# Performance work log

Hardware: AMD Instinct MI355X
Metric: run time of the kernel (lower is better)

## Reference

```python
import jax, jax.numpy as jnp
import numpy as np

B, T, D, H = 4, 2048, 1024, 16
DH = D // H          # 64
HALF = DH // 2       # 32


def _rope_tables(T, half, base=10000.0):
    inv_freq = 1.0 / (base ** (np.arange(half, dtype=np.float32) / half))
    t = np.arange(T, dtype=np.float32)
    ang = np.outer(t, inv_freq)                       # [T, half]
    cos = jnp.asarray(np.cos(ang))[None, None]        # [1,1,T,half]
    sin = jnp.asarray(np.sin(ang))[None, None]
    return cos, sin


def setup_inputs() -> dict:
    key = jax.random.key(0)
    kx, kq, kp = jax.random.split(key, 3)
    cos, sin = _rope_tables(T, HALF)
    return {
        "x": jax.random.normal(kx, (B, T, D), dtype=jnp.float32),
        "cos": cos,
        "sin": sin,
        "W_qkv": jax.random.normal(kq, (3 * D, D), dtype=jnp.float32) * (D ** -0.5),
        "W_proj": jax.random.normal(kp, (D, D), dtype=jnp.float32) * (D ** -0.5),
    }


def _apply_rope(q, k, cos, sin):
    # q,k: [B,H,T,dh]; cos,sin: [1,1,T,dh/2]
    t = q.shape[2]
    c, s = cos[:, :, :t, :], sin[:, :, :t, :]
    h = q.shape[-1] // 2
    q1, q2 = q[..., :h], q[..., h:]
    k1, k2 = k[..., :h], k[..., h:]
    q_rot = jnp.concatenate([q1 * c - q2 * s, q1 * s + q2 * c], axis=-1)
    k_rot = jnp.concatenate([k1 * c - k2 * s, k1 * s + k2 * c], axis=-1)
    return q_rot, k_rot


def reference(x, cos, sin, W_qkv, W_proj):
    Bb, Tt, C = x.shape
    qkv = x @ W_qkv.T                                 # [B,T,3C]
    q, k, v = jnp.split(qkv, 3, axis=2)
    # [B,T,C] -> [B,H,T,dh]
    q = q.reshape(Bb, Tt, H, DH).transpose(0, 2, 1, 3)
    k = k.reshape(Bb, Tt, H, DH).transpose(0, 2, 1, 3)
    v = v.reshape(Bb, Tt, H, DH).transpose(0, 2, 1, 3)
    q, k = _apply_rope(q, k, cos, sin)
    w = jnp.einsum("bhqd,bhkd->bhqk", q, k) * (DH ** -0.5)
    causal = jnp.tril(jnp.ones((Tt, Tt), dtype=bool))
    w = jnp.where(causal, w, -jnp.inf)
    w = jax.nn.softmax(w.astype(jnp.float32), axis=-1).astype(x.dtype)
    out = jnp.einsum("bhqk,bhkd->bhqd", w, v)
    # XSA: subtract self-value contribution (diagonal attention weight)
    self_w = jnp.diagonal(w, axis1=-2, axis2=-1)[..., None]  # [B,H,T,1]
    out = out - self_w * v
    out = out.transpose(0, 2, 1, 3).reshape(Bb, Tt, C)
    return out @ W_proj.T
```

## Files before the change

kernel.cpp:

```cpp
#include <hip/hip_runtime.h>

constexpr int Tq = 2048;
constexpr int Dq = 1024;

typedef __bf16 bf16x8 __attribute__((ext_vector_type(8)));
typedef float f32x4 __attribute__((ext_vector_type(4)));
typedef _Float16 f16;
typedef f16 f16x4 __attribute__((ext_vector_type(4)));
typedef f16 f16x8v __attribute__((ext_vector_type(8)));
typedef unsigned short u16;
typedef u16 u16x4 __attribute__((ext_vector_type(4)));
typedef u16 u16x8 __attribute__((ext_vector_type(8)));

__device__ __forceinline__ u16 f2bf(float f) {
    unsigned int u = __float_as_uint(f);
    u += 0x7fffu + ((u >> 16) & 1u);
    return (u16)(u >> 16);
}
__device__ __forceinline__ float bf2f(u16 h) {
    return __uint_as_float(((unsigned int)h) << 16);
}

__device__ __forceinline__ void gld_lds16(const void* g, void* l) {
    __builtin_amdgcn_global_load_lds(
        (const __attribute__((address_space(1))) unsigned int*)g,
        (__attribute__((address_space(3))) unsigned int*)l, 16, 0, 0);
}

__global__ void cvt3_f32_bf16(const float* __restrict__ a, u16* __restrict__ oa, int na,
                              const float* __restrict__ b, u16* __restrict__ ob, int nb,
                              const float* __restrict__ c, u16* __restrict__ oc, int nc) {
    int i = blockIdx.x * 256 + threadIdx.x;
    const float* in; u16* out;
    if (i < na) { in = a; out = oa; }
    else if (i < na + nb) { in = b; out = ob; i -= na; }
    else if (i < na + nb + nc) { in = c; out = oc; i -= na + nb; }
    else return;
    float4 v = ((const float4*)in)[i];
    u16x4 o;
    o.x = f2bf(v.x); o.y = f2bf(v.y); o.z = f2bf(v.z); o.w = f2bf(v.w);
    ((u16x4*)out)[i] = o;
}

template <int OUT_F32>
__global__ __launch_bounds__(256) void gemm_bt(const u16* __restrict__ A,
                                               const u16* __restrict__ B,
                                               void* __restrict__ Cv,
                                               int M, int N, int K) {
    __shared__ u16 As[128 * 32];
    __shared__ u16 Bs[128 * 32];
    const int t = threadIdx.x;
    const int lane = t & 63;
    const int wave = t >> 6;
    const int l16 = lane & 15;
    const int quad = lane >> 4;
    const int bm = blockIdx.x * 128;
    const int bn = blockIdx.y * 128;
    const int wm = (wave & 1) * 64;
    const int wn = (wave >> 1) * 64;
    const int srow = t >> 2;
    const int scol = (t & 3) * 8;

    f32x4 acc[4][4] = {};

    const u16* Ab = A + (size_t)(bm + srow) * K + scol;
    const u16* Bb = B + (size_t)(bn + srow) * K + scol;

    for (int k0 = 0; k0 < K; k0 += 32) {
        gld_lds16(Ab + k0,                    (char*)As + t * 16);
        gld_lds16(Ab + (size_t)64 * K + k0,   (char*)As + 4096 + t * 16);
        gld_lds16(Bb + k0,                    (char*)Bs + t * 16);
        gld_lds16(Bb + (size_t)64 * K + k0,   (char*)Bs + 4096 + t * 16);
        __syncthreads();

        bf16x8 af[4], bf[4];
#pragma unroll
        for (int i = 0; i < 4; i++) {
            af[i] = *(const bf16x8*)&As[(wm + i * 16 + l16) * 32 + quad * 8];
            bf[i] = *(const bf16x8*)&Bs[(wn + i * 16 + l16) * 32 + quad * 8];
        }
#pragma unroll
        for (int i = 0; i < 4; i++)
#pragma unroll
            for (int j = 0; j < 4; j++)
                acc[i][j] = __builtin_amdgcn_mfma_f32_16x16x32_bf16(af[i], bf[j], acc[i][j], 0, 0, 0);
        __syncthreads();
    }

#pragma unroll
    for (int i = 0; i < 4; i++)
#pragma unroll
        for (int j = 0; j < 4; j++)
#pragma unroll
            for (int r = 0; r < 4; r++) {
                const int gm = bm + wm + i * 16 + quad * 4 + r;
                const int gn = bn + wn + j * 16 + l16;
                if (OUT_F32)
                    ((float*)Cv)[(size_t)gm * N + gn] = acc[i][j][r];
                else
                    ((u16*)Cv)[(size_t)gm * N + gn] = f2bf(acc[i][j][r]);
            }
}

__global__ __launch_bounds__(256) void rope_scatter(const u16* __restrict__ qkv,
                                                    const float* __restrict__ cosT,
                                                    const float* __restrict__ sinT,
                                                    u16* __restrict__ Qb,
                                                    u16* __restrict__ Kb,
                                                    f16* __restrict__ Vtg) {
    __shared__ f16 Vt[64 * 64];
    const int tid = threadIdx.x;
    const int i = blockIdx.x;
    const int xcd = i & 7, w = i >> 3;
    const int bh = xcd * 8 + (w >> 5);
    const int b = bh >> 4, h = bh & 15;
    const int t0 = (w & 31) * 64;
    const int tloc = tid >> 2;
    const int p = tid & 3;
    const int ta = t0 + tloc;
    const size_t rowb = ((size_t)b * Tq + ta) * (3 * Dq) + h * 64;
    const int lo = (p & 1) * 16;

    union U16 { u16x8 v[2]; u16 a[16]; };
    U16 qlo, qhi, klo, khi, vv;
    qlo.v[0] = *(const u16x8*)(qkv + rowb + lo);
    qlo.v[1] = *(const u16x8*)(qkv + rowb + lo + 8);
    qhi.v[0] = *(const u16x8*)(qkv + rowb + lo + 32);
    qhi.v[1] = *(const u16x8*)(qkv + rowb + lo + 40);
    klo.v[0] = *(const u16x8*)(qkv + rowb + Dq + lo);
    klo.v[1] = *(const u16x8*)(qkv + rowb + Dq + lo + 8);
    khi.v[0] = *(const u16x8*)(qkv + rowb + Dq + lo + 32);
    khi.v[1] = *(const u16x8*)(qkv + rowb + Dq + lo + 40);
    vv.v[0]  = *(const u16x8*)(qkv + rowb + 2 * Dq + p * 16);
    vv.v[1]  = *(const u16x8*)(qkv + rowb + 2 * Dq + p * 16 + 8);

    float cc[16], ss[16];
    {
        const float4* c4 = (const float4*)(cosT + (size_t)ta * 32 + lo);
        const float4* s4 = (const float4*)(sinT + (size_t)ta * 32 + lo);
#pragma unroll
        for (int e = 0; e < 4; e++) {
            float4 c = c4[e], s = s4[e];
            cc[e * 4 + 0] = c.x; cc[e * 4 + 1] = c.y; cc[e * 4 + 2] = c.z; cc[e * 4 + 3] = c.w;
            ss[e * 4 + 0] = s.x; ss[e * 4 + 1] = s.y; ss[e * 4 + 2] = s.z; ss[e * 4 + 3] = s.w;
        }
    }

    U16 qo, ko;
    const bool first = (p < 2);
#pragma unroll
    for (int e = 0; e < 16; e++) {
        const float q1 = bf2f(qlo.a[e]), q2 = bf2f(qhi.a[e]);
        const float k1 = bf2f(klo.a[e]), k2 = bf2f(khi.a[e]);
        const float qv = first ? (q1 * cc[e] - q2 * ss[e]) : (q1 * ss[e] + q2 * cc[e]);
        const float kv = first ? (k1 * cc[e] - k2 * ss[e]) : (k1 * ss[e] + k2 * cc[e]);
        qo.a[e] = f2bf(qv * 0.18033688011112042f);
        ko.a[e] = f2bf(kv);
    }
    const size_t qrow = ((size_t)bh * Tq + ta) * 64 + p * 16;
    *(u16x8*)(Qb + qrow)     = qo.v[0];
    *(u16x8*)(Qb + qrow + 8) = qo.v[1];
    *(u16x8*)(Kb + qrow)     = ko.v[0];
    *(u16x8*)(Kb + qrow + 8) = ko.v[1];

#pragma unroll
    for (int e = 0; e < 16; e++) {
        const int d = p * 16 + e;
        const int pc = (tloc >> 3) ^ ((d + (d >> 4)) & 7);
        Vt[d * 64 + pc * 8 + (tloc & 7)] = (f16)bf2f(vv.a[e]);
    }
    __syncthreads();
    const int drow = tid >> 2, tseg = tid & 3;
    const int rot = (drow + (drow >> 4)) & 7;
    f16x8v r0 = *(const f16x8v*)&Vt[drow * 64 + ((2 * tseg) ^ rot) * 8];
    f16x8v r1 = *(const f16x8v*)&Vt[drow * 64 + ((2 * tseg + 1) ^ rot) * 8];
    f16* vout = Vtg + ((size_t)bh * 64 + drow) * Tq + t0 + tseg * 16;
    *(f16x8v*)vout = r0;
    *(f16x8v*)(vout + 8) = r1;
}

template <bool MASK>
__device__ __forceinline__ void flash_tile(const u16* __restrict__ Ks,
                                           const f16* __restrict__ Vs,
                                           const bf16x8& qf0, const bf16x8& qf1,
                                           int l16, int quad, int i_loc,
                                           float& l_run, f32x4* o_acc) {
    f32x4 s[4];
    const int cp0 = quad ^ (l16 & 7);
    const int cp1 = (4 + quad) ^ (l16 & 7);
#pragma unroll
    for (int tn = 0; tn < 4; tn++) {
        const int jrow = tn * 16 + l16;
        bf16x8 kf0 = *(const bf16x8*)&Ks[jrow * 64 + cp0 * 8];
        bf16x8 kf1 = *(const bf16x8*)&Ks[jrow * 64 + cp1 * 8];
        f32x4 z = {0.f, 0.f, 0.f, 0.f};
        z = __builtin_amdgcn_mfma_f32_16x16x32_bf16(kf0, qf0, z, 0, 0, 0);
        z = __builtin_amdgcn_mfma_f32_16x16x32_bf16(kf1, qf1, z, 0, 0, 0);
        s[tn] = z;
    }
    float rsa[4];
#pragma unroll
    for (int tn = 0; tn < 4; tn++) {
        float rs = 0.f;
#pragma unroll
        for (int r = 0; r < 4; r++) {
            float v = s[tn][r];
            if (MASK) {
                const int j_loc = tn * 16 + quad * 4 + r;
                if (j_loc > i_loc) v = -1e30f;
            }
            float p = exp2f(v);
            rs += p;
            if (MASK) {
                const int j_loc = tn * 16 + quad * 4 + r;
                if (j_loc == i_loc) p = 0.f;
            }
            s[tn][r] = p;
        }
        rsa[tn] = rs;
    }
    l_run += (rsa[0] + rsa[1]) + (rsa[2] + rsa[3]);

    f16x4 pf[4];
#pragma unroll
    for (int tk = 0; tk < 4; tk++)
        pf[tk] = f16x4{(f16)s[tk][0], (f16)s[tk][1], (f16)s[tk][2], (f16)s[tk][3]};
#pragma unroll
    for (int td = 0; td < 4; td++) {
        const int drow = td * 16 + l16;
#pragma unroll
        for (int tk = 0; tk < 4; tk++) {
            const int cp = (2 * tk + (quad >> 1)) ^ (l16 & 7);
            f16x4 vf = *(const f16x4*)&Vs[drow * 64 + cp * 8 + (quad & 1) * 4];
            o_acc[td] = __builtin_amdgcn_mfma_f32_16x16x16f16(vf, pf[tk], o_acc[td], 0, 0, 0);
        }
    }
}

__global__ __launch_bounds__(512, 4) void flash(const u16* __restrict__ Qb,
                                                const u16* __restrict__ Kb,
                                                const f16* __restrict__ Vtg,
                                                u16* __restrict__ Ob) {
    __shared__ __align__(16) char smem[65536];

    const int t = threadIdx.x, lane = t & 63, wave = t >> 6;
    const int l16 = lane & 15, quad = lane >> 4;
    const int i = blockIdx.x;
    const int xcd = i & 7, w = i >> 3;
    const int bh = xcd * 8 + (w >> 4);
    const int b = bh >> 4, h = bh & 15;
    const int x = w & 15;
    const int qt = (wave < 4) ? x : (31 - x);
    const int q0w = qt * 64;
    const u16* Qp = Qb + (size_t)bh * Tq * 64;
    const u16* Kp = Kb + (size_t)bh * Tq * 64;
    const f16* Vp = Vtg + (size_t)bh * 64 * Tq;

    const int i_abs = q0w + (wave & 3) * 16 + l16;
    bf16x8 qf0 = *(const bf16x8*)(Qp + (size_t)i_abs * 64 + quad * 8);
    bf16x8 qf1 = *(const bf16x8*)(Qp + (size_t)i_abs * 64 + 32 + quad * 8);
    asm volatile("s_waitcnt vmcnt(0)" : "+v"(qf0), "+v"(qf1) :: "memory");

    float l_run = 0.f;
    f32x4 o_acc[4] = {};

    const int srow = t >> 3;
    const int sc = (t & 7) ^ (srow & 7);
    const int diag_n = qt;
    const int i_tloc = (wave & 3) * 16 + l16;
    const int nt = 32 - x;

    auto stage = [&](int n) {
        const int j0 = n * 64;
        char* buf = smem + (n & 3) * 16384;
        gld_lds16(Kp + (size_t)(j0 + srow) * 64 + sc * 8, buf + t * 16);
        gld_lds16(Vp + (size_t)srow * Tq + j0 + sc * 8,   buf + 8192 + t * 16);
    };

    stage(0);
    stage(1);
    for (int n = 0; n < nt; n++) {
        char* cur = smem + (n & 3) * 16384;
        if (n + 2 < nt) {
            stage(n + 2);
            asm volatile("s_waitcnt vmcnt(4)\n\ts_barrier" ::: "memory");
        } else if (n + 1 < nt) {
            asm volatile("s_waitcnt vmcnt(2)\n\ts_barrier" ::: "memory");
        } else {
            asm volatile("s_waitcnt vmcnt(0)\n\ts_barrier" ::: "memory");
        }
        const u16* Ks = (const u16*)cur;
        const f16* Vs = (const f16*)(cur + 8192);
        if (n < diag_n)
            flash_tile<false>(Ks, Vs, qf0, qf1, l16, quad, i_tloc, l_run, o_acc);
        else if (n == diag_n)
            flash_tile<true>(Ks, Vs, qf0, qf1, l16, quad, i_tloc, l_run, o_acc);
    }

    l_run += __shfl_xor(l_run, 16, 64);
    l_run += __shfl_xor(l_run, 32, 64);
    const float inv_l = 1.f / l_run;

    __syncthreads();
    u16* Os = (u16*)smem;
#pragma unroll
    for (int td = 0; td < 4; td++) {
        u16x4 o;
#pragma unroll
        for (int r = 0; r < 4; r++) o[r] = f2bf(o_acc[td][r] * inv_l);
        *(u16x4*)&Os[wave * 1152 + l16 * 72 + td * 16 + quad * 4] = o;
    }
    __syncthreads();
    const int oi = lane >> 2, od = (lane & 3) * 16;
    u16x8 r0 = *(const u16x8*)&Os[wave * 1152 + oi * 72 + od];
    u16x8 r1 = *(const u16x8*)&Os[wave * 1152 + oi * 72 + od + 8];
    const size_t orow = ((size_t)b * Tq + q0w + (wave & 3) * 16 + oi) * Dq + h * 64 + od;
    *(u16x8*)&Ob[orow] = r0;
    *(u16x8*)&Ob[orow + 8] = r1;
}

extern "C" void kernel_launch(void* const* d_in, const int* in_sizes, int n_in,
                              void* d_out, int out_size, void* d_ws, size_t ws_size,
                              hipStream_t stream) {
    const float* x     = (const float*)d_in[0];
    const float* cosT  = (const float*)d_in[1];
    const float* sinT  = (const float*)d_in[2];
    const float* Wqkv  = (const float*)d_in[3];
    const float* Wproj = (const float*)d_in[4];

    u16* xb     = (u16*)d_ws;
    u16* wqkvb  = xb + (size_t)8192 * 1024;
    u16* wprojb = wqkvb + (size_t)3072 * 1024;
    u16* qkv    = wprojb + (size_t)1024 * 1024;
    u16* Qb     = qkv + (size_t)8192 * 3072;
    u16* Kb     = Qb + (size_t)64 * 2048 * 64;
    f16* Vtg    = (f16*)(Kb + (size_t)64 * 2048 * 64);
    u16* attn   = qkv;

    cvt3_f32_bf16<<<12288, 256, 0, stream>>>(x, xb, 2097152,
                                             Wqkv, wqkvb, 786432,
                                             Wproj, wprojb, 262144);

    gemm_bt<0><<<dim3(64, 24), 256, 0, stream>>>(xb, wqkvb, (void*)qkv, 8192, 3072, 1024);
    rope_scatter<<<2048, 256, 0, stream>>>(qkv, cosT, sinT, Qb, Kb, Vtg);
    flash<<<1024, 512, 0, stream>>>(Qb, Kb, Vtg, attn);
    gemm_bt<1><<<dim3(64, 8), 256, 0, stream>>>(attn, wprojb, d_out, 8192, 1024, 1024);
}
```

Measured before the change: 277.6 us.

## Fuse RoPE and Q/K/V head scatter into QKV GEMM epilogue

Removes the intermediate bf16 qkv buffer and the separate rope_scatter kernel by applying RoPE, the Q scale, and the head-major/transposed V layout directly in the QKV GEMM epilogue. This avoids a full write and read-back of the 8192x3072 activation and one kernel launch. In exchange, epilogue stores become narrower and more scattered (2-byte Q/K stores, 8-byte strided V stores), and the cos/sin loads are per-element rather than vectorised.

```diff
diff --git a/kernel.cpp b/kernel.cpp
--- a/kernel.cpp
+++ b/kernel.cpp
@@ -7,7 +7,6 @@
 typedef float f32x4 __attribute__((ext_vector_type(4)));
 typedef _Float16 f16;
 typedef f16 f16x4 __attribute__((ext_vector_type(4)));
-typedef f16 f16x8v __attribute__((ext_vector_type(8)));
 typedef unsigned short u16;
 typedef u16 u16x4 __attribute__((ext_vector_type(4)));
 typedef u16 u16x8 __attribute__((ext_vector_type(8)));
@@ -16,9 +15,6 @@
     unsigned int u = __float_as_uint(f);
     u += 0x7fffu + ((u >> 16) & 1u);
     return (u16)(u >> 16);
-}
-__device__ __forceinline__ float bf2f(u16 h) {
-    return __uint_as_float(((unsigned int)h) << 16);
 }
 
 __device__ __forceinline__ void gld_lds16(const void* g, void* l) {
@@ -42,10 +38,99 @@
     ((u16x4*)out)[i] = o;
 }
 
-template <int OUT_F32>
+__global__ __launch_bounds__(256) void gemm_qkv(const u16* __restrict__ A,
+                                                const u16* __restrict__ B,
+                                                const float* __restrict__ cosT,
+                                                const float* __restrict__ sinT,
+                                                u16* __restrict__ Qb,
+                                                u16* __restrict__ Kb,
+                                                f16* __restrict__ Vtg) {
+    constexpr int K = 1024, N = 3072;
+    __shared__ u16 As[128 * 32];
+    __shared__ u16 Bs[128 * 32];
+    const int t = threadIdx.x;
+    const int lane = t & 63;
+    const int wave = t >> 6;
+    const int l16 = lane & 15;
+    const int quad = lane >> 4;
+    const int bm = blockIdx.x * 128;
+    const int by = blockIdx.y;
+    const int bn = by * 128;
+    const int wm = (wave & 1) * 64;
+    const int wn = (wave >> 1) * 64;
+    const int srow = t >> 2;
+    const int scol = (t & 3) * 8;
+
+    f32x4 acc[4][4] = {};
+
+    const u16* Ab = A + (size_t)(bm + srow) * K + scol;
+    const u16* Bb = B + (size_t)(bn + srow) * K + scol;
+
+    for (int k0 = 0; k0 < K; k0 += 32) {
+        gld_lds16(Ab + k0,                    (char*)As + t * 16);
+        gld_lds16(Ab + (size_t)64 * K + k0,   (char*)As + 4096 + t * 16);
+        gld_lds16(Bb + k0,                    (char*)Bs + t * 16);
+        gld_lds16(Bb + (size_t)64 * K + k0,   (char*)Bs + 4096 + t * 16);
+        __syncthreads();
+
+        bf16x8 af[4], bf[4];
+#pragma unroll
+        for (int i = 0; i < 4; i++) {
+            af[i] = *(const bf16x8*)&As[(wm + i * 16 + l16) * 32 + quad * 8];
+            bf[i] = *(const bf16x8*)&Bs[(wn + i * 16 + l16) * 32 + quad * 8];
+        }
+#pragma unroll
+        for (int i = 0; i < 4; i++)
+#pragma unroll
+            for (int j = 0; j < 4; j++)
+                acc[i][j] = __builtin_amdgcn_mfma_f32_16x16x32_bf16(af[i], bf[j], acc[i][j], 0, 0, 0);
+        __syncthreads();
+    }
+
+    const int kind = by >> 3;
+    if (kind < 2) {
+        u16* Out = kind ? Kb : Qb;
+        const float qscale = kind ? 1.f : 0.18033688011112042f;
+        const int h = ((by & 7) << 1) + (wn >> 6);
+#pragma unroll
+        for (int i = 0; i < 4; i++)
+#pragma unroll
+            for (int r = 0; r < 4; r++) {
+                const int gm = bm + wm + i * 16 + quad * 4 + r;
+                const int b = gm >> 11, tt = gm & 2047;
+                const size_t row = ((size_t)(b * 16 + h) * Tq + tt) * 64;
+#pragma unroll
+                for (int jj = 0; jj < 2; jj++) {
+                    const int dd = jj * 16 + l16;
+                    const float c = cosT[tt * 32 + dd];
+                    const float s = sinT[tt * 32 + dd];
+                    const float v1 = acc[i][jj][r];
+                    const float v2 = acc[i][jj + 2][r];
+                    Out[row + dd]      = f2bf((v1 * c - v2 * s) * qscale);
+                    Out[row + dd + 32] = f2bf((v1 * s + v2 * c) * qscale);
+                }
+            }
+    } else {
+#pragma unroll
+        for (int i = 0; i < 4; i++) {
+            const int gm0 = bm + wm + i * 16 + quad * 4;
+            const int b = gm0 >> 11, tt = gm0 & 2047;
+#pragma unroll
+            for (int j = 0; j < 4; j++) {
+                const int col = wn + j * 16 + l16;
+                const int h = ((by & 7) << 1) + (col >> 6);
+                const int d = col & 63;
+                f16x4 o = {(f16)acc[i][j][0], (f16)acc[i][j][1],
+                           (f16)acc[i][j][2], (f16)acc[i][j][3]};
+                *(f16x4*)&Vtg[((size_t)(b * 16 + h) * 64 + d) * Tq + tt] = o;
+            }
+        }
+    }
+}
+
 __global__ __launch_bounds__(256) void gemm_bt(const u16* __restrict__ A,
                                                const u16* __restrict__ B,
-                                               void* __restrict__ Cv,
+                                               float* __restrict__ Cv,
                                                int M, int N, int K) {
     __shared__ u16 As[128 * 32];
     __shared__ u16 Bs[128 * 32];
@@ -95,88 +180,8 @@
             for (int r = 0; r < 4; r++) {
                 const int gm = bm + wm + i * 16 + quad * 4 + r;
                 const int gn = bn + wn + j * 16 + l16;
-                if (OUT_F32)
-                    ((float*)Cv)[(size_t)gm * N + gn] = acc[i][j][r];
-                else
-                    ((u16*)Cv)[(size_t)gm * N + gn] = f2bf(acc[i][j][r]);
-            }
-}
-
-__global__ __launch_bounds__(256) void rope_scatter(const u16* __restrict__ qkv,
-                                                    const float* __restrict__ cosT,
-                                                    const float* __restrict__ sinT,
-                                                    u16* __restrict__ Qb,
-                                                    u16* __restrict__ Kb,
-                                                    f16* __restrict__ Vtg) {
-    __shared__ f16 Vt[64 * 64];
-    const int tid = threadIdx.x;
-    const int i = blockIdx.x;
-    const int xcd = i & 7, w = i >> 3;
-    const int bh = xcd * 8 + (w >> 5);
-    const int b = bh >> 4, h = bh & 15;
-    const int t0 = (w & 31) * 64;
-    const int tloc = tid >> 2;
-    const int p = tid & 3;
-    const int ta = t0 + tloc;
-    const size_t rowb = ((size_t)b * Tq + ta) * (3 * Dq) + h * 64;
-    const int lo = (p & 1) * 16;
-
-    union U16 { u16x8 v[2]; u16 a[16]; };
-    U16 qlo, qhi, klo, khi, vv;
-    qlo.v[0] = *(const u16x8*)(qkv + rowb + lo);
-    qlo.v[1] = *(const u16x8*)(qkv + rowb + lo + 8);
-    qhi.v[0] = *(const u16x8*)(qkv + rowb + lo + 32);
-    qhi.v[1] = *(const u16x8*)(qkv + rowb + lo + 40);
-    klo.v[0] = *(const u16x8*)(qkv + rowb + Dq + lo);
-    klo.v[1] = *(const u16x8*)(qkv + rowb + Dq + lo + 8);
-    khi.v[0] = *(const u16x8*)(qkv + rowb + Dq + lo + 32);
-    khi.v[1] = *(const u16x8*)(qkv + rowb + Dq + lo + 40);
-    vv.v[0]  = *(const u16x8*)(qkv + rowb + 2 * Dq + p * 16);
-    vv.v[1]  = *(const u16x8*)(qkv + rowb + 2 * Dq + p * 16 + 8);
-
-    float cc[16], ss[16];
-    {
-        const float4* c4 = (const float4*)(cosT + (size_t)ta * 32 + lo);
-        const float4* s4 = (const float4*)(sinT + (size_t)ta * 32 + lo);
-#pragma unroll
-        for (int e = 0; e < 4; e++) {
-            float4 c = c4[e], s = s4[e];
-            cc[e * 4 + 0] = c.x; cc[e * 4 + 1] = c.y; cc[e * 4 + 2] = c.z; cc[e * 4 + 3] = c.w;
-            ss[e * 4 + 0] = s.x; ss[e * 4 + 1] = s.y; ss[e * 4 + 2] = s.z; ss[e * 4 + 3] = s.w;
-        }
-    }
-
-    U16 qo, ko;
-    const bool first = (p < 2);
-#pragma unroll
-    for (int e = 0; e < 16; e++) {
-        const float q1 = bf2f(qlo.a[e]), q2 = bf2f(qhi.a[e]);
-        const float k1 = bf2f(klo.a[e]), k2 = bf2f(khi.a[e]);
-        const float qv = first ? (q1 * cc[e] - q2 * ss[e]) : (q1 * ss[e] + q2 * cc[e]);
-        const float kv = first ? (k1 * cc[e] - k2 * ss[e]) : (k1 * ss[e] + k2 * cc[e]);
-        qo.a[e] = f2bf(qv * 0.18033688011112042f);
-        ko.a[e] = f2bf(kv);
-    }
-    const size_t qrow = ((size_t)bh * Tq + ta) * 64 + p * 16;
-    *(u16x8*)(Qb + qrow)     = qo.v[0];
-    *(u16x8*)(Qb + qrow + 8) = qo.v[1];
-    *(u16x8*)(Kb + qrow)     = ko.v[0];
-    *(u16x8*)(Kb + qrow + 8) = ko.v[1];
-
-#pragma unroll
-    for (int e = 0; e < 16; e++) {
-        const int d = p * 16 + e;
-        const int pc = (tloc >> 3) ^ ((d + (d >> 4)) & 7);
-        Vt[d * 64 + pc * 8 + (tloc & 7)] = (f16)bf2f(vv.a[e]);
-    }
-    __syncthreads();
-    const int drow = tid >> 2, tseg = tid & 3;
-    const int rot = (drow + (drow >> 4)) & 7;
-    f16x8v r0 = *(const f16x8v*)&Vt[drow * 64 + ((2 * tseg) ^ rot) * 8];
-    f16x8v r1 = *(const f16x8v*)&Vt[drow * 64 + ((2 * tseg + 1) ^ rot) * 8];
-    f16* vout = Vtg + ((size_t)bh * 64 + drow) * Tq + t0 + tseg * 16;
-    *(f16x8v*)vout = r0;
-    *(f16x8v*)(vout + 8) = r1;
+                Cv[(size_t)gm * N + gn] = acc[i][j][r];
+            }
 }
 
 template <bool MASK>
@@ -331,18 +336,16 @@
     u16* xb     = (u16*)d_ws;
     u16* wqkvb  = xb + (size_t)8192 * 1024;
     u16* wprojb = wqkvb + (size_t)3072 * 1024;
-    u16* qkv    = wprojb + (size_t)1024 * 1024;
-    u16* Qb     = qkv + (size_t)8192 * 3072;
+    u16* Qb     = wprojb + (size_t)1024 * 1024;
     u16* Kb     = Qb + (size_t)64 * 2048 * 64;
     f16* Vtg    = (f16*)(Kb + (size_t)64 * 2048 * 64);
-    u16* attn   = qkv;
+    u16* attn   = (u16*)(Vtg + (size_t)64 * 64 * 2048);
 
     cvt3_f32_bf16<<<12288, 256, 0, stream>>>(x, xb, 2097152,
                                              Wqkv, wqkvb, 786432,
                                              Wproj, wprojb, 262144);
 
-    gemm_bt<0><<<dim3(64, 24), 256, 0, stream>>>(xb, wqkvb, (void*)qkv, 8192, 3072, 1024);
-    rope_scatter<<<2048, 256, 0, stream>>>(qkv, cosT, sinT, Qb, Kb, Vtg);
+    gemm_qkv<<<dim3(64, 24), 256, 0, stream>>>(xb, wqkvb, cosT, sinT, Qb, Kb, Vtg);
     flash<<<1024, 512, 0, stream>>>(Qb, Kb, Vtg, attn);
-    gemm_bt<1><<<dim3(64, 8), 256, 0, stream>>>(attn, wprojb, d_out, 8192, 1024, 1024);
-}
+    gemm_bt<<<dim3(64, 8), 256, 0, stream>>>(attn, wprojb, (float*)d_out, 8192, 1024, 1024);
+}
```

Result: faster. 255.6 us (-7.9%).
